# Optimization experiments

Measured on AMD Instinct MI355X. Metric: run time of the kernel, lower is better.

Reference implementation:

```python
import jax, jax.numpy as jnp
import numpy as np

KRYLOV_DIM = 8
T_END = 1.0
EPS = 1e-12


def setup_inputs() -> dict:
    key = jax.random.key(0)
    k1, k2, k3 = jax.random.split(key, 3)
    B, C, H, Wd = 8, 256, 64, 64
    s0 = jax.random.uniform(k1, (B, C, H, Wd), dtype=jnp.float32)
    v = jax.random.normal(k2, (B, C, H, Wd), dtype=jnp.float32)
    W = jax.random.normal(k3, (C, C), dtype=jnp.float32) / np.float32(np.sqrt(C))
    return {"s0": s0, "v": v, "W": W}


def reference(s0, v, W):
    # fitness: learned channel-mixing linear operator (1x1-conv style)
    def fitness(x):
        return jnp.einsum('oc,bchw->bohw', W, x)

    # replicator vector field R_{s}[x] = s*x - s * sum_c(s*x)
    def replicator(s, x):
        sx = s * x
        return sx - s * jnp.sum(sx, axis=1, keepdims=True)

    A = lambda x: fitness(replicator(s0, x))
    dot = lambda a, b: jnp.sum(a * b, axis=(1, 2, 3))  # batched inner product

    m = KRYLOV_DIM
    B = v.shape[0]

    # ---- Arnoldi iteration (batched, modified Gram-Schmidt) ----
    vnorm = jnp.sqrt(dot(v, v))  # [B]
    Q = [v / vnorm[:, None, None, None]]
    Hcols = []
    for k in range(m):
        w = A(Q[k])
        col = []
        for j in range(k + 1):
            h = dot(Q[j], w)               # [B]
            col.append(h)
            w = w - h[:, None, None, None] * Q[j]
        hnext = jnp.sqrt(dot(w, w))        # subdiagonal entry
        Q.append(w / (hnext + EPS)[:, None, None, None])
        col.append(hnext)
        col += [jnp.zeros_like(hnext)] * (m - k - 1)  # pad column to m+1 rows
        Hcols.append(jnp.stack(col, axis=-1))          # [B, m+1]
    Hmat = jnp.stack(Hcols, axis=-1)  # [B, m+1, m]
    T = Hmat[:, :m, :]                # square upper-Hessenberg [B, m, m]

    # ---- extended matrix + batched small matrix exponential ----
    ext = jnp.zeros((B, m + 1, m + 1), dtype=T.dtype)
    ext = ext.at[:, :m, :m].set(T_END * T)
    ext = ext.at[:, 0, m].set(T_END)
    expm_ext = jax.scipy.linalg.expm(ext)   # batched over leading dim
    coords = expm_ext[:, :m, -1]            # [B, m] Krylov coordinates

    # ---- fused weighted sum of Krylov vectors ----
    Qstack = jnp.stack(Q[:m], axis=0)       # [m, B, C, H, W]
    v_end = jnp.einsum('bj,jbchw->bchw', coords, Qstack)
    return v_end * vnorm[:, None, None, None]
```

## Files before the change

kernel.cpp:

```cpp
#include <hip/hip_runtime.h>
#include <math.h>

#define Bn   8
#define Cn   256
#define HWn  4096
#define FB   (Cn * HWn)
#define NTOT (Bn * FB)
#define TEND 1.0
#define EPSK 1e-12f
#define NT   64
#define RS   40
#define WTS  68

typedef float f32x4 __attribute__((ext_vector_type(4)));
typedef short bf16x8 __attribute__((ext_vector_type(8)));

__device__ inline float b2f(unsigned int u) {
    return __uint_as_float(u << 16);
}
__device__ inline unsigned short f2b(float f) {
    unsigned u = __float_as_uint(f);
    unsigned r = u + 0x7FFFu + ((u >> 16) & 1u);
    return (unsigned short)(r >> 16);
}


__global__ void init_kernel(float* __restrict__ p) {
    for (int i = threadIdx.x; i < 1024; i += 256) p[i] = 0.0f;
}

__global__ void wsplit_kernel(const float* __restrict__ W,
                              unsigned short* __restrict__ Whs,
                              unsigned short* __restrict__ Wls) {
    int kc = blockIdx.x, mt = blockIdx.y, l = threadIdx.x;
    int m = mt * 16 + (l & 15);
    int k0 = kc * 32 + (l >> 4) * 8;
#pragma unroll
    for (int j = 0; j < 8; ++j) {
        float wv = W[m * 256 + k0 + j];
        unsigned short h = f2b(wv);
        unsigned short lo = f2b(wv - b2f(h));
        int idx = ((kc * 16 + mt) * 64 + l) * 8 + j;
        Whs[idx] = h; Wls[idx] = lo;
    }
}

template <int K>
__global__ __launch_bounds__(256, 2) void step_kernel(
        const float* __restrict__ v, const float* __restrict__ s0,
        const unsigned short* __restrict__ Whs, const unsigned short* __restrict__ Wls,
        unsigned short* __restrict__ Qb, float* __restrict__ acc,
        float* __restrict__ w,
        unsigned short* __restrict__ Zh, unsigned short* __restrict__ Zl) {
    __shared__ __align__(16) char smem_u[34816];
    short* Ph0 = (short*)smem_u;
    short* Ph1 = (short*)(smem_u + 5120);
    short* Pl0 = (short*)(smem_u + 10240);
    short* Pl1 = (short*)(smem_u + 15360);
    float* wt  = (float*)smem_u;
    __shared__ float tred[4][64];
    __shared__ float ts[NT];
    __shared__ float nred[4];
    __shared__ float dred[4][8];

    const int tid = threadIdx.x;
    const int b = blockIdx.y;
    const int sbase = blockIdx.x * NT;
    const size_t boff = (size_t)b * FB;
    const int lane = tid & 63, wvi = tid >> 6;
    const int mbase = wvi * 64;
    const int ch8 = wvi * 8;
    const int p   = lane;

    float cj[K > 0 ? K : 1];
    if (K > 0) {
        float mm[K > 0 ? K : 1];
        mm[0] = sqrtf(acc[512 + b]);
#pragma unroll
        for (int j = 1; j < K; ++j) mm[j] = sqrtf(acc[512 + j * 8 + b]) + EPSK * mm[j - 1];
#pragma unroll
        for (int j = 0; j < K; ++j)
            cj[j] = acc[((K - 1) * 8 + j) * 8 + b] / (mm[j] * mm[j]);
    }
    unsigned short* QK = Qb + (size_t)(K > 0 ? K - 1 : 0) * NTOT;

    float tp = 0.f, np = 0.f;

    auto stage = [&](int kc, int bb) {
        const int c0 = kc * 32 + ch8;
        const size_t off = boff + (size_t)c0 * HWn + sbase + p;
        short* ph = bb ? Ph1 : Ph0;
        short* pl = bb ? Pl1 : Pl0;
        bf16x8 hv, lv;
#pragma unroll
        for (int e = 0; e < 8; ++e) {
            const size_t oe = off + (size_t)e * HWn;
            float s = s0[oe];
            float pe;
            if (K < 0) {
                pe = s;
            } else if (K == 0) {
                float xv = v[oe];
                np = fmaf(xv, xv, np);
                tp = fmaf(xv, s, tp);
                pe = s * xv;
            } else {
                float xe = w[oe];
                xe = fmaf(-cj[0], v[oe], xe);
#pragma unroll
                for (int j = 1; j < K; ++j)
                    xe = fmaf(-cj[j], b2f(Qb[(size_t)(j - 1) * NTOT + oe]), xe);
                unsigned short hx = f2b(xe);
                QK[oe] = hx;
                float xr = b2f(hx);
                np = fmaf(xr, xr, np);
                tp = fmaf(xr, s, tp);
                pe = s * xr;
            }
            unsigned short h = f2b(pe);
            hv[e] = (short)h;
            lv[e] = (short)f2b(pe - b2f(h));
        }
        *(bf16x8*)(ph + p * RS + ch8) = hv;
        *(bf16x8*)(pl + p * RS + ch8) = lv;
    };

    f32x4 ac[4][4];
#pragma unroll
    for (int i = 0; i < 4; ++i)
#pragma unroll
        for (int j = 0; j < 4; ++j) ac[i][j] = (f32x4){0.f, 0.f, 0.f, 0.f};

    stage(0, 0);
    for (int kc = 0; kc < 8; ++kc) {
        __syncthreads();
        if (kc < 7) stage(kc + 1, (kc + 1) & 1);
        const short* ph = (kc & 1) ? Ph1 : Ph0;
        const short* pl = (kc & 1) ? Pl1 : Pl0;
        bf16x8 ah[4], al[4], bh[4], bl[4];
#pragma unroll
        for (int rt = 0; rt < 4; ++rt) {
            int mt = (mbase >> 4) + rt;
            ah[rt] = *(const bf16x8*)(Whs + (size_t)kc * 8192 + (mt * 64 + lane) * 8);
            al[rt] = *(const bf16x8*)(Wls + (size_t)kc * 8192 + (mt * 64 + lane) * 8);
        }
#pragma unroll
        for (int ct = 0; ct < 4; ++ct) {
            int n = ct * 16 + (lane & 15);
            int k8 = (lane >> 4) * 8;
            bh[ct] = *(const bf16x8*)(ph + n * RS + k8);
            bl[ct] = *(const bf16x8*)(pl + n * RS + k8);
        }
#pragma unroll
        for (int rt = 0; rt < 4; ++rt)
#pragma unroll
            for (int ct = 0; ct < 4; ++ct) {
                ac[rt][ct] = __builtin_amdgcn_mfma_f32_16x16x32_bf16(ah[rt], bh[ct], ac[rt][ct], 0, 0, 0);
                ac[rt][ct] = __builtin_amdgcn_mfma_f32_16x16x32_bf16(ah[rt], bl[ct], ac[rt][ct], 0, 0, 0);
                ac[rt][ct] = __builtin_amdgcn_mfma_f32_16x16x32_bf16(al[rt], bh[ct], ac[rt][ct], 0, 0, 0);
            }
    }

    __syncthreads();
    if (K >= 0) {
        tred[wvi][p] = tp;
        float q = np;
        for (int off2 = 32; off2 > 0; off2 >>= 1) q += __shfl_down(q, off2);
        if (lane == 0) nred[wvi] = q;
    }
    __syncthreads();
    if (K >= 0) {
        if (tid < NT)
            ts[tid] = tred[0][tid] + tred[1][tid] + tred[2][tid] + tred[3][tid];
        if (tid == 0)
            atomicAdd(&acc[512 + K * 8 + b], nred[0] + nred[1] + nred[2] + nred[3]);
    }

    float dp[K >= 0 ? K + 1 : 1];
#pragma unroll
    for (int j = 0; j < (K >= 0 ? K + 1 : 1); ++j) dp[j] = 0.f;
#pragma unroll
    for (int g = 0; g < 2; ++g) {
        __syncthreads();
        if ((wvi >> 1) == g) {
            int rl = (wvi & 1) * 64;
#pragma unroll
            for (int rt = 0; rt < 4; ++rt)
#pragma unroll
                for (int ct = 0; ct < 4; ++ct) {
                    int r0 = rl + rt * 16 + (lane >> 4) * 4;
                    int ccol = ct * 16 + (lane & 15);
#pragma unroll
                    for (int reg = 0; reg < 4; ++reg)
                        wt[(r0 + reg) * WTS + ccol] = ac[rt][ct][reg];
                }
        }
        __syncthreads();
#pragma unroll
        for (int rr = 0; rr < 8; ++rr) {
            int rlocal = rr * 16 + (tid >> 4);
            int rabs = g * 128 + rlocal;
            int col = (tid & 15) * 4;
            const float* src = wt + rlocal * WTS + col;
            float4 wv4 = {src[0], src[1], src[2], src[3]};
            size_t idx = boff + (size_t)rabs * HWn + sbase + col;
            if (K < 0) {
                ushort4 zh4, zl4;
                unsigned short h0 = f2b(wv4.x), h1 = f2b(wv4.y);
                unsigned short h2 = f2b(wv4.z), h3 = f2b(wv4.w);
                zh4.x = h0; zh4.y = h1; zh4.z = h2; zh4.w = h3;
                zl4.x = f2b(wv4.x - b2f(h0)); zl4.y = f2b(wv4.y - b2f(h1));
                zl4.z = f2b(wv4.z - b2f(h2)); zl4.w = f2b(wv4.w - b2f(h3));
                *(ushort4*)(Zh + idx) = zh4;
                *(ushort4*)(Zl + idx) = zl4;
            } else {
                ushort4 zh4 = *(const ushort4*)(Zh + idx);
                ushort4 zl4 = *(const ushort4*)(Zl + idx);
                float z0 = b2f(zh4.x) + b2f(zl4.x), z1 = b2f(zh4.y) + b2f(zl4.y);
                float z2 = b2f(zh4.z) + b2f(zl4.z), z3 = b2f(zh4.w) + b2f(zl4.w);
                float4 wf;
                wf.x = wv4.x - z0 * ts[col + 0];
                wf.y = wv4.y - z1 * ts[col + 1];
                wf.z = wv4.z - z2 * ts[col + 2];
                wf.w = wv4.w - z3 * ts[col + 3];
                *(float4*)(w + idx) = wf;
                float4 vv4 = *(const float4*)(v + idx);
                dp[0] = fmaf(wf.x, vv4.x, dp[0]);
                dp[0] = fmaf(wf.y, vv4.y, dp[0]);
                dp[0] = fmaf(wf.z, vv4.z, dp[0]);
                dp[0] = fmaf(wf.w, vv4.w, dp[0]);
#pragma unroll
                for (int j = 1; j <= (K >= 0 ? K : 0); ++j) {
                    ushort4 u = *(const ushort4*)(Qb + (size_t)(j - 1) * NTOT + idx);
                    dp[j] = fmaf(wf.x, b2f(u.x), dp[j]);
                    dp[j] = fmaf(wf.y, b2f(u.y), dp[j]);
                    dp[j] = fmaf(wf.z, b2f(u.z), dp[j]);
                    dp[j] = fmaf(wf.w, b2f(u.w), dp[j]);
                }
            }
        }
    }
    if (K >= 0) {
#pragma unroll
        for (int j = 0; j <= K; ++j) {
            float q = dp[j];
            for (int off2 = 32; off2 > 0; off2 >>= 1) q += __shfl_down(q, off2);
            if (lane == 0) dred[wvi][j] = q;
        }
        __syncthreads();
        if (tid <= K)
            atomicAdd(&acc[(K * 8 + tid) * 8 + b],
                      dred[0][tid] + dred[1][tid] + dred[2][tid] + dred[3][tid]);
    }
}

__global__ __launch_bounds__(128) void expm_kernel(const float* __restrict__ acc,
                                                   float* __restrict__ coordsOut) {
    __shared__ double Am[81], Pm[81], Tm[81];
    __shared__ double ssc;
    __shared__ int sn;
    const int b = blockIdx.x;
    const int t = threadIdx.x;
    const int r = t / 9, c = t % 9;
    double m[8];
    m[0] = sqrt((double)acc[512 + b]);
    for (int j = 1; j < 8; ++j) m[j] = sqrt((double)acc[512 + j * 8 + b]) + 1e-12 * m[j - 1];
    if (t < 81) {
        double val = 0.0;
        if (r < 8 && c < 8) {
            if (r <= c) val = TEND * (double)acc[(c * 8 + r) * 8 + b] / (m[r] * m[c]);
            else if (r == c + 1) val = TEND * sqrt((double)acc[512 + r * 8 + b]) / m[c];
        }
        if (r == 0 && c == 8) val = TEND;
        Am[t] = val;
    }
    __syncthreads();
    if (t == 0) {
        double mx = 0.0;
        for (int rr = 0; rr < 9; ++rr) {
            double s = 0.0;
            for (int cc = 0; cc < 9; ++cc) s += fabs(Am[rr * 9 + cc]);
            if (s > mx) mx = s;
        }
        int n = 0;
        while (mx > 0.25 && n < 48) { mx *= 0.5; ++n; }
        double sc = 1.0;
        for (int ii = 0; ii < n; ++ii) sc *= 0.5;
        sn = n; ssc = sc;
    }
    __syncthreads();
    if (t < 81) Am[t] *= ssc;
    __syncthreads();
    if (t < 81) Pm[t] = (r == c) ? 1.0 : 0.0;
    __syncthreads();
    for (int i = 20; i >= 1; --i) {
        if (t < 81) {
            double s = 0.0;
            for (int k = 0; k < 9; ++k) s += Am[r * 9 + k] * Pm[k * 9 + c];
            Tm[t] = ((r == c) ? 1.0 : 0.0) + s / (double)i;
        }
        __syncthreads();
        if (t < 81) Pm[t] = Tm[t];
        __syncthreads();
    }
    int n = sn;
    for (int q = 0; q < n; ++q) {
        if (t < 81) {
            double s = 0.0;
            for (int k = 0; k < 9; ++k) s += Pm[r * 9 + k] * Pm[k * 9 + c];
            Tm[t] = s;
        }
        __syncthreads();
        if (t < 81) Pm[t] = Tm[t];
        __syncthreads();
    }
    if (t < 8) coordsOut[b * 8 + t] = (float)(Pm[t * 9 + 8] * m[0] / m[t]);
}

__device__ inline void unp8(uint4 u, float* f) {
    f[0] = b2f(u.x & 0xFFFFu); f[1] = b2f(u.x >> 16);
    f[2] = b2f(u.y & 0xFFFFu); f[3] = b2f(u.y >> 16);
    f[4] = b2f(u.z & 0xFFFFu); f[5] = b2f(u.z >> 16);
    f[6] = b2f(u.w & 0xFFFFu); f[7] = b2f(u.w >> 16);
}

__global__ __launch_bounds__(256) void combine_kernel(const unsigned short* __restrict__ Qb,
                                                      const float* __restrict__ v,
                                                      const float* __restrict__ coords,
                                                      float* __restrict__ out) {
    int b = blockIdx.y;
    const size_t boff = (size_t)b * FB;
    float cf[8];
#pragma unroll
    for (int j = 0; j < 8; ++j) cf[j] = coords[b * 8 + j];
    const float4* vv = (const float4*)(v + boff);
    const uint4* uv[8];
#pragma unroll
    for (int j = 1; j < 8; ++j)
        uv[j] = (const uint4*)(Qb + (size_t)(j - 1) * NTOT + boff);
    int i = blockIdx.x * 256 + threadIdx.x;
    float4* ov = (float4*)(out + boff);
#pragma unroll
    for (int r = 0; r < 2; ++r) {
        int idx = i + r * 65536;
        float4 v0 = vv[2 * idx], v1 = vv[2 * idx + 1];
        float a[8] = {cf[0] * v0.x, cf[0] * v0.y, cf[0] * v0.z, cf[0] * v0.w,
                      cf[0] * v1.x, cf[0] * v1.y, cf[0] * v1.z, cf[0] * v1.w};
#pragma unroll
        for (int j = 1; j < 8; ++j) {
            uint4 u = uv[j][idx];
            float ue[8]; unp8(u, ue);
#pragma unroll
            for (int e = 0; e < 8; ++e) a[e] = fmaf(cf[j], ue[e], a[e]);
        }
        float4 o0 = {a[0], a[1], a[2], a[3]};
        float4 o1 = {a[4], a[5], a[6], a[7]};
        ov[2 * idx] = o0; ov[2 * idx + 1] = o1;
    }
}

extern "C" void kernel_launch(void* const* d_in, const int* in_sizes, int n_in,
                              void* d_out, int out_size, void* d_ws, size_t ws_size,
                              hipStream_t stream) {
    const float* s0 = (const float*)d_in[0];
    const float* v  = (const float*)d_in[1];
    const float* W  = (const float*)d_in[2];
    float* out = (float*)d_out;

    float* ws     = (float*)d_ws;
    float* acc    = ws;
    float* coords = ws + 576;
    unsigned short* Whs = (unsigned short*)(ws + 1024);
    unsigned short* Wls = Whs + 65536;
    unsigned short* Zh  = (unsigned short*)(ws + 1024 + 65536);
    unsigned short* Zl  = Zh + NTOT;
    unsigned short* Qb  = Zh + 2 * (size_t)NTOT;
    float* w      = out;

    init_kernel<<<dim3(1), dim3(256), 0, stream>>>(ws);
    wsplit_kernel<<<dim3(8, 16), dim3(64), 0, stream>>>(W, Whs, Wls);

    dim3 ga(64, 8), blk(256);
    step_kernel<-1><<<ga, blk, 0, stream>>>(v, s0, Whs, Wls, Qb, acc, w, Zh, Zl);
#define STEPK(K) step_kernel<K><<<ga, blk, 0, stream>>>(v, s0, Whs, Wls, Qb, acc, w, Zh, Zl);
    STEPK(0) STEPK(1) STEPK(2) STEPK(3) STEPK(4) STEPK(5) STEPK(6) STEPK(7)
#undef STEPK

    expm_kernel<<<dim3(8), dim3(128), 0, stream>>>(acc, coords);
    combine_kernel<<<dim3(256, 8), blk, 0, stream>>>(Qb, v, coords, out);
}
```

Baseline: 579.1 us.

## Split step kernel output channels across two blocks and vectorize staging loads

Each step kernel block now computes only half of the 256 output channels. The grid doubles to 128x8 blocks, the register accumulators halve, shared memory shrinks and launch bounds rise to 4 blocks per CU. Input staging is rewritten to use float4/ushort4 loads, and each thread packs two channels per LDS write. Both channel halves recompute the full staged operand, so global reads of s0/v/w/Qb are duplicated, hopefully absorbed by cache. Only the first half writes the new Krylov vector and the norm contribution.

Measured after the change: 531.5 us. 8.2% less time.

```diff
diff --git a/kernel.cpp b/kernel.cpp
--- a/kernel.cpp
+++ b/kernel.cpp
@@ -46,31 +46,32 @@
 }
 
 template <int K>
-__global__ __launch_bounds__(256, 2) void step_kernel(
+__global__ __launch_bounds__(256, 4) void step_kernel(
         const float* __restrict__ v, const float* __restrict__ s0,
         const unsigned short* __restrict__ Whs, const unsigned short* __restrict__ Wls,
         unsigned short* __restrict__ Qb, float* __restrict__ acc,
         float* __restrict__ w,
         unsigned short* __restrict__ Zh, unsigned short* __restrict__ Zl) {
-    __shared__ __align__(16) char smem_u[34816];
+    __shared__ __align__(16) char smem_u[20480];
     short* Ph0 = (short*)smem_u;
     short* Ph1 = (short*)(smem_u + 5120);
     short* Pl0 = (short*)(smem_u + 10240);
     short* Pl1 = (short*)(smem_u + 15360);
     float* wt  = (float*)smem_u;
-    __shared__ float tred[4][64];
+    __shared__ float tred[16][WTS];
     __shared__ float ts[NT];
     __shared__ float nred[4];
     __shared__ float dred[4][8];
 
     const int tid = threadIdx.x;
     const int b = blockIdx.y;
-    const int sbase = blockIdx.x * NT;
+    const int mhalf = blockIdx.x >> 6;
+    const int sbase = (blockIdx.x & 63) * NT;
     const size_t boff = (size_t)b * FB;
     const int lane = tid & 63, wvi = tid >> 6;
-    const int mbase = wvi * 64;
-    const int ch8 = wvi * 8;
-    const int p   = lane;
+    const int mbase = mhalf * 128 + wvi * 32;
+    const int c2 = tid >> 4;
+    const int pos4 = (tid & 15) * 4;
 
     float cj[K > 0 ? K : 1];
     if (K > 0) {
@@ -84,50 +85,79 @@
     }
     unsigned short* QK = Qb + (size_t)(K > 0 ? K - 1 : 0) * NTOT;
 
-    float tp = 0.f, np = 0.f;
+    float tp[4] = {0.f, 0.f, 0.f, 0.f};
+    float np = 0.f;
 
     auto stage = [&](int kc, int bb) {
-        const int c0 = kc * 32 + ch8;
-        const size_t off = boff + (size_t)c0 * HWn + sbase + p;
+        const int c0 = kc * 32 + 2 * c2;
+        const size_t offA = boff + (size_t)c0 * HWn + sbase + pos4;
         short* ph = bb ? Ph1 : Ph0;
         short* pl = bb ? Pl1 : Pl0;
-        bf16x8 hv, lv;
-#pragma unroll
-        for (int e = 0; e < 8; ++e) {
-            const size_t oe = off + (size_t)e * HWn;
-            float s = s0[oe];
-            float pe;
+        float pA[4], pB[4];
+#pragma unroll
+        for (int h = 0; h < 2; ++h) {
+            const size_t oe = offA + (size_t)h * HWn;
+            float4 s4 = *(const float4*)(s0 + oe);
+            float se[4] = {s4.x, s4.y, s4.z, s4.w};
+            float* pr = h ? pB : pA;
             if (K < 0) {
-                pe = s;
+#pragma unroll
+                for (int i = 0; i < 4; ++i) pr[i] = se[i];
             } else if (K == 0) {
-                float xv = v[oe];
-                np = fmaf(xv, xv, np);
-                tp = fmaf(xv, s, tp);
-                pe = s * xv;
+                float4 x4 = *(const float4*)(v + oe);
+                float xe[4] = {x4.x, x4.y, x4.z, x4.w};
+#pragma unroll
+                for (int i = 0; i < 4; ++i) {
+                    if (mhalf == 0) np = fmaf(xe[i], xe[i], np);
+                    tp[i] = fmaf(xe[i], se[i], tp[i]);
+                    pr[i] = se[i] * xe[i];
+                }
             } else {
-                float xe = w[oe];
-                xe = fmaf(-cj[0], v[oe], xe);
-#pragma unroll
-                for (int j = 1; j < K; ++j)
-                    xe = fmaf(-cj[j], b2f(Qb[(size_t)(j - 1) * NTOT + oe]), xe);
-                unsigned short hx = f2b(xe);
-                QK[oe] = hx;
-                float xr = b2f(hx);
-                np = fmaf(xr, xr, np);
-                tp = fmaf(xr, s, tp);
-                pe = s * xr;
+                float4 w4 = *(const float4*)(w + oe);
+                float4 v4 = *(const float4*)(v + oe);
+                float xe[4];
+                xe[0] = fmaf(-cj[0], v4.x, w4.x);
+                xe[1] = fmaf(-cj[0], v4.y, w4.y);
+                xe[2] = fmaf(-cj[0], v4.z, w4.z);
+                xe[3] = fmaf(-cj[0], v4.w, w4.w);
+#pragma unroll
+                for (int j = 1; j < K; ++j) {
+                    ushort4 u = *(const ushort4*)(Qb + (size_t)(j - 1) * NTOT + oe);
+                    xe[0] = fmaf(-cj[j], b2f(u.x), xe[0]);
+                    xe[1] = fmaf(-cj[j], b2f(u.y), xe[1]);
+                    xe[2] = fmaf(-cj[j], b2f(u.z), xe[2]);
+                    xe[3] = fmaf(-cj[j], b2f(u.w), xe[3]);
+                }
+                unsigned int h0 = f2b(xe[0]), h1 = f2b(xe[1]);
+                unsigned int h2 = f2b(xe[2]), h3 = f2b(xe[3]);
+                if (mhalf == 0) {
+                    ushort4 o;
+                    o.x = (unsigned short)h0; o.y = (unsigned short)h1;
+                    o.z = (unsigned short)h2; o.w = (unsigned short)h3;
+                    *(ushort4*)(QK + oe) = o;
+                }
+                float xr[4] = {b2f(h0), b2f(h1), b2f(h2), b2f(h3)};
+#pragma unroll
+                for (int i = 0; i < 4; ++i) {
+                    if (mhalf == 0) np = fmaf(xr[i], xr[i], np);
+                    tp[i] = fmaf(xr[i], se[i], tp[i]);
+                    pr[i] = se[i] * xr[i];
+                }
             }
-            unsigned short h = f2b(pe);
-            hv[e] = (short)h;
-            lv[e] = (short)f2b(pe - b2f(h));
-        }
-        *(bf16x8*)(ph + p * RS + ch8) = hv;
-        *(bf16x8*)(pl + p * RS + ch8) = lv;
+        }
+#pragma unroll
+        for (int i = 0; i < 4; ++i) {
+            unsigned hA = f2b(pA[i]), hB = f2b(pB[i]);
+            unsigned lA = f2b(pA[i] - b2f((unsigned short)hA));
+            unsigned lB = f2b(pB[i] - b2f((unsigned short)hB));
+            *(unsigned*)(ph + (pos4 + i) * RS + 2 * c2) = hA | (hB << 16);
+            *(unsigned*)(pl + (pos4 + i) * RS + 2 * c2) = lA | (lB << 16);
+        }
     };
 
-    f32x4 ac[4][4];
-#pragma unroll
-    for (int i = 0; i < 4; ++i)
+    f32x4 ac[2][4];
+#pragma unroll
+    for (int i = 0; i < 2; ++i)
 #pragma unroll
         for (int j = 0; j < 4; ++j) ac[i][j] = (f32x4){0.f, 0.f, 0.f, 0.f};
 
@@ -137,9 +167,9 @@
         if (kc < 7) stage(kc + 1, (kc + 1) & 1);
         const short* ph = (kc & 1) ? Ph1 : Ph0;
         const short* pl = (kc & 1) ? Pl1 : Pl0;
-        bf16x8 ah[4], al[4], bh[4], bl[4];
-#pragma unroll
-        for (int rt = 0; rt < 4; ++rt) {
+        bf16x8 ah[2], al[2], bh[4], bl[4];
+#pragma unroll
+        for (int rt = 0; rt < 2; ++rt) {
             int mt = (mbase >> 4) + rt;
             ah[rt] = *(const bf16x8*)(Whs + (size_t)kc * 8192 + (mt * 64 + lane) * 8);
             al[rt] = *(const bf16x8*)(Wls + (size_t)kc * 8192 + (mt * 64 + lane) * 8);
@@ -152,7 +182,7 @@
             bl[ct] = *(const bf16x8*)(pl + n * RS + k8);
         }
 #pragma unroll
-        for (int rt = 0; rt < 4; ++rt)
+        for (int rt = 0; rt < 2; ++rt)
 #pragma unroll
             for (int ct = 0; ct < 4; ++ct) {
                 ac[rt][ct] = __builtin_amdgcn_mfma_f32_16x16x32_bf16(ah[rt], bh[ct], ac[rt][ct], 0, 0, 0);
@@ -163,16 +193,22 @@
 
     __syncthreads();
     if (K >= 0) {
-        tred[wvi][p] = tp;
-        float q = np;
-        for (int off2 = 32; off2 > 0; off2 >>= 1) q += __shfl_down(q, off2);
-        if (lane == 0) nred[wvi] = q;
+        *(float4*)(&tred[c2][pos4]) = *(float4*)tp;
+        if (mhalf == 0) {
+            float q = np;
+            for (int off2 = 32; off2 > 0; off2 >>= 1) q += __shfl_down(q, off2);
+            if (lane == 0) nred[wvi] = q;
+        }
     }
     __syncthreads();
     if (K >= 0) {
-        if (tid < NT)
-            ts[tid] = tred[0][tid] + tred[1][tid] + tred[2][tid] + tred[3][tid];
-        if (tid == 0)
+        if (tid < NT) {
+            float s = 0.f;
+#pragma unroll
+            for (int g = 0; g < 16; ++g) s += tred[g][tid];
+            ts[tid] = s;
+        }
+        if (tid == 0 && mhalf == 0)
             atomicAdd(&acc[512 + K * 8 + b], nred[0] + nred[1] + nred[2] + nred[3]);
     }
 
@@ -183,9 +219,9 @@
     for (int g = 0; g < 2; ++g) {
         __syncthreads();
         if ((wvi >> 1) == g) {
-            int rl = (wvi & 1) * 64;
-#pragma unroll
-            for (int rt = 0; rt < 4; ++rt)
+            int rl = (wvi & 1) * 32;
+#pragma unroll
+            for (int rt = 0; rt < 2; ++rt)
 #pragma unroll
                 for (int ct = 0; ct < 4; ++ct) {
                     int r0 = rl + rt * 16 + (lane >> 4) * 4;
@@ -197,9 +233,9 @@
         }
         __syncthreads();
 #pragma unroll
-        for (int rr = 0; rr < 8; ++rr) {
+        for (int rr = 0; rr < 4; ++rr) {
             int rlocal = rr * 16 + (tid >> 4);
-            int rabs = g * 128 + rlocal;
+            int rabs = mhalf * 128 + g * 64 + rlocal;
             int col = (tid & 15) * 4;
             const float* src = wt + rlocal * WTS + col;
             float4 wv4 = {src[0], src[1], src[2], src[3]};
@@ -380,7 +416,7 @@
     init_kernel<<<dim3(1), dim3(256), 0, stream>>>(ws);
     wsplit_kernel<<<dim3(8, 16), dim3(64), 0, stream>>>(W, Whs, Wls);
 
-    dim3 ga(64, 8), blk(256);
+    dim3 ga(128, 8), blk(256);
     step_kernel<-1><<<ga, blk, 0, stream>>>(v, s0, Whs, Wls, Qb, acc, w, Zh, Zl);
 #define STEPK(K) step_kernel<K><<<ga, blk, 0, stream>>>(v, s0, Whs, Wls, Qb, acc, w, Zh, Zl);
     STEPK(0) STEPK(1) STEPK(2) STEPK(3) STEPK(4) STEPK(5) STEPK(6) STEPK(7)
```
